# Kernel optimization log

Measured on AMD Instinct MI355X. Metric: run time of the kernel, lower is better.

## Reference

```python
import jax, jax.numpy as jnp
import numpy as np

NUM_VOXELS = 1_000_000
N_POINTS = 1_500_000
TOTAL_PROP_PTS = 1_000_000
NUM_PROPOSALS = 2048
IN_CH = 134  # 3 + 3 + 128
M = 16       # backbone output width
BATCH = 8


def setup_inputs() -> dict:
    key = jax.random.key(0)
    k1, k2, k3, k4, k5, k6 = jax.random.split(key, 6)
    voxel_feats = jax.random.normal(k1, (NUM_VOXELS, IN_CH), dtype=jnp.float32)
    W = jax.random.normal(k2, (IN_CH, M), dtype=jnp.float32) * 0.05
    p2v_map = jax.random.randint(k3, (N_POINTS,), 0, NUM_VOXELS, dtype=jnp.int64)
    # column 0: proposal id (unused), column 1: point index into pt_feats
    col1 = jax.random.randint(k4, (TOTAL_PROP_PTS,), 0, N_POINTS, dtype=jnp.int64)
    gt_proposals_idx = jnp.stack([jnp.zeros_like(col1), col1], axis=1)
    interior = jnp.sort(jax.random.randint(k5, (NUM_PROPOSALS - 1,), 0, TOTAL_PROP_PTS, dtype=jnp.int64))
    gt_proposals_offset = jnp.concatenate([
        jnp.zeros((1,), jnp.int64), interior,
        jnp.full((1,), TOTAL_PROP_PTS, jnp.int64)])
    # column 0 is the batch (scene) id
    locs_scaled = jax.random.randint(k6, (N_POINTS, 4), 0, BATCH, dtype=jnp.int32)
    return {
        'voxel_feats': voxel_feats,
        'W': W,
        'p2v_map': p2v_map,
        'gt_proposals_idx': gt_proposals_idx,
        'gt_proposals_offset': gt_proposals_offset,
        'locs_scaled': locs_scaled,
    }


def reference(voxel_feats, W, p2v_map, gt_proposals_idx, gt_proposals_offset, locs_scaled):
    # Stand-in for the Minkowski sparse backbone: pointwise projection + ReLU, 134 -> 16.
    feats = jax.nn.relu(voxel_feats @ W)                 # (V, 16)
    pt_feats = feats[p2v_map]                            # (N, 16) voxel->point gather

    P = gt_proposals_offset.shape[0] - 1
    point_idx = gt_proposals_idx[:, 1]                   # (T,)
    T = point_idx.shape[0]

    # CSR offsets -> segment ids (replaces the Python loop over proposals)
    seg_ids = jnp.searchsorted(gt_proposals_offset, jnp.arange(T), side='right') - 1

    gathered = pt_feats[point_idx]                       # (T, 16) ragged gather
    sums = jax.ops.segment_sum(gathered, seg_ids, num_segments=P)
    counts = jax.ops.segment_sum(jnp.ones((T,), feats.dtype), seg_ids, num_segments=P)
    proposal_feats = sums / jnp.maximum(counts, 1.0)[:, None]   # (P, 16) segment mean

    batch_idxs = locs_scaled[:, 0]                       # (N,) scene ids
    proposals_batchId = batch_idxs[point_idx][gt_proposals_offset[:-1]]  # (P,)
    proposal_objectness_scores = jnp.ones((P,), dtype=bool)
    return proposal_feats, proposals_batchId, proposal_objectness_scores
```

## Files before the change

### kernel.cpp

```cpp
#include <hip/hip_runtime.h>

#define NUM_VOXELS     1000000
#define N_POINTS       1500000
#define TOTAL_PROP_PTS 1000000
#define NUM_PROPOSALS  2048
#define IN_CH          134
#define M_OUT          16

typedef unsigned int  uint;
typedef unsigned short ushort;

__device__ __forceinline__ ushort f2bf(float f) {
    uint u = __float_as_uint(f);
    uint r = (u + 0x7FFFu + ((u >> 16) & 1u)) >> 16;
    return (ushort)r;
}

__global__ void k_zero_flags(uint* __restrict__ flags4) {
    int i = blockIdx.x * 256 + threadIdx.x;
    if (i < NUM_VOXELS / 4) flags4[i] = 0;
}

__global__ void k_set_flags(const int* __restrict__ prop_idx,
                            const int* __restrict__ p2v,
                            unsigned char* __restrict__ flags) {
    int t = blockIdx.x * 256 + threadIdx.x;
    if (t < TOTAL_PROP_PTS) {
        int p = prop_idx[2 * t + 1];
        flags[p2v[p]] = 1;
    }
}

__global__ __launch_bounds__(256, 2) void k_gemm_relu(
    const float* __restrict__ A, const float* __restrict__ W,
    const unsigned char* __restrict__ flags,
    uint* __restrict__ featsb)
{
    __shared__ float lds[4][64 * 65];
    const int wave = threadIdx.x >> 6;
    const int lane = threadIdx.x & 63;
    const int v0   = blockIdx.x * 256 + wave * 64;
    if (v0 >= NUM_VOXELS) return;

    const int myflag = flags[v0 + lane];

    float* chunk = lds[wave];
    float acc[M_OUT];
#pragma unroll
    for (int c = 0; c < M_OUT; ++c) acc[c] = 0.f;

    for (int kc = 0; kc < IN_CH; kc += 64) {
        const int KC = (IN_CH - kc) >= 64 ? 64 : (IN_CH - kc);
        if (KC == 64) {
            const int half = lane >> 5;
            const int c2   = (lane & 31) * 2;
#pragma unroll 8
            for (int j = 0; j < 32; ++j) {
                const int row = j * 2 + half;
                const int rf  = __shfl(myflag, row, 64);
                if (rf) {
                    const float2 val = *(const float2*)(A + (size_t)(v0 + row) * IN_CH + kc + c2);
                    chunk[row * 65 + c2]     = val.x;
                    chunk[row * 65 + c2 + 1] = val.y;
                }
            }
        } else {
#pragma unroll
            for (int j = 0; j < 6; ++j) {
                const int e   = j * 64 + lane;
                const int row = e / 6;
                const int col = e - row * 6;
                const int rf  = __shfl(myflag, row, 64);
                if (rf) chunk[row * 65 + col] = A[(size_t)(v0 + row) * IN_CH + kc + col];
            }
        }
        const float* wbase = W + kc * M_OUT;
        for (int kk = 0; kk < KC; ++kk) {
            const float a = chunk[lane * 65 + kk];
            const float* wr = wbase + kk * M_OUT;
#pragma unroll
            for (int c = 0; c < M_OUT; ++c) acc[c] = fmaf(a, wr[c], acc[c]);
        }
    }

    if (myflag) {
        uint u[8];
#pragma unroll
        for (int i = 0; i < 8; ++i) {
            const float lo = fmaxf(acc[2 * i],     0.f);
            const float hi = fmaxf(acc[2 * i + 1], 0.f);
            u[i] = (uint)f2bf(lo) | ((uint)f2bf(hi) << 16);
        }
        uint4* orow = (uint4*)(featsb + (size_t)(v0 + lane) * 8);
        orow[0] = make_uint4(u[0], u[1], u[2], u[3]);
        orow[1] = make_uint4(u[4], u[5], u[6], u[7]);
    }
}

__global__ __launch_bounds__(256) void k_propmean(
    const uint*  __restrict__ featsb,
    const int*   __restrict__ p2v,
    const int*   __restrict__ prop_idx,
    const int*   __restrict__ offsets,
    const int*   __restrict__ locs,
    float*       __restrict__ out)
{
    const int s   = blockIdx.x;
    const int tid = threadIdx.x;
    const int t0  = offsets[s];
    const int t1  = offsets[s + 1];

    float acc[M_OUT];
#pragma unroll
    for (int c = 0; c < M_OUT; ++c) acc[c] = 0.f;

    for (int t = t0 + tid; t < t1; t += 256) {
        const int p = prop_idx[2 * t + 1];
        const int v = p2v[p];
        const uint4* fp = (const uint4*)(featsb + (size_t)v * 8);
        const uint4 q0 = fp[0], q1 = fp[1];
        const uint u[8] = {q0.x, q0.y, q0.z, q0.w, q1.x, q1.y, q1.z, q1.w};
#pragma unroll
        for (int i = 0; i < 8; ++i) {
            acc[2 * i]     += __uint_as_float(u[i] << 16);
            acc[2 * i + 1] += __uint_as_float(u[i] & 0xFFFF0000u);
        }
    }

#pragma unroll
    for (int c = 0; c < M_OUT; ++c) {
#pragma unroll
        for (int off = 32; off > 0; off >>= 1)
            acc[c] += __shfl_down(acc[c], off, 64);
    }

    __shared__ float red[4][M_OUT];
    const int lane = tid & 63, wv = tid >> 6;
    if (lane == 0) {
#pragma unroll
        for (int c = 0; c < M_OUT; ++c) red[wv][c] = acc[c];
    }
    __syncthreads();

    if (tid < M_OUT) {
        const float sum = red[0][tid] + red[1][tid] + red[2][tid] + red[3][tid];
        const float cnt = (float)(t1 - t0);
        out[s * M_OUT + tid] = sum / fmaxf(cnt, 1.f);
    }
    if (tid == 0) {
        const int p = prop_idx[2 * t0 + 1];
        out[NUM_PROPOSALS * M_OUT + s]                 = (float)locs[4 * p];
        out[NUM_PROPOSALS * M_OUT + NUM_PROPOSALS + s] = 1.0f;
    }
}

extern "C" void kernel_launch(void* const* d_in, const int* in_sizes, int n_in,
                              void* d_out, int out_size, void* d_ws, size_t ws_size,
                              hipStream_t stream)
{
    const float* A    = (const float*)d_in[0];
    const float* W    = (const float*)d_in[1];
    const int*   p2v  = (const int*)  d_in[2];
    const int*   pidx = (const int*)  d_in[3];
    const int*   offs = (const int*)  d_in[4];
    const int*   locs = (const int*)  d_in[5];
    float*       out  = (float*)      d_out;

    uint*          featsb = (uint*)d_ws;
    unsigned char* flags  = (unsigned char*)d_ws + (size_t)NUM_VOXELS * 32;

    k_zero_flags<<<(NUM_VOXELS / 4 + 255) / 256, 256, 0, stream>>>((uint*)flags);
    k_set_flags<<<(TOTAL_PROP_PTS + 255) / 256, 256, 0, stream>>>(pidx, p2v, flags);
    k_gemm_relu<<<(NUM_VOXELS + 255) / 256, 256, 0, stream>>>(A, W, flags, featsb);
    k_propmean<<<NUM_PROPOSALS, 256, 0, stream>>>(featsb, p2v, pidx, offs, locs, out);
}
```

Baseline: 940.1 us.

## Compact flagged voxels and compute GEMM per-thread rows without LDS staging

Result: no change. 931.3 us (-0.9%).

```diff
diff --git a/kernel.cpp b/kernel.cpp
--- a/kernel.cpp
+++ b/kernel.cpp
@@ -7,7 +7,7 @@
 #define IN_CH          134
 #define M_OUT          16
 
-typedef unsigned int  uint;
+typedef unsigned int   uint;
 typedef unsigned short ushort;
 
 __device__ __forceinline__ ushort f2bf(float f) {
@@ -16,9 +16,10 @@
     return (ushort)r;
 }
 
-__global__ void k_zero_flags(uint* __restrict__ flags4) {
+__global__ void k_zero(uint* __restrict__ flags4, int* __restrict__ count) {
     int i = blockIdx.x * 256 + threadIdx.x;
     if (i < NUM_VOXELS / 4) flags4[i] = 0;
+    if (i == 0) *count = 0;
 }
 
 __global__ void k_set_flags(const int* __restrict__ prop_idx,
@@ -31,59 +32,66 @@
     }
 }
 
-__global__ __launch_bounds__(256, 2) void k_gemm_relu(
+__global__ __launch_bounds__(256) void k_compact(
+    const unsigned char* __restrict__ flags,
+    int* __restrict__ ids, int* __restrict__ count)
+{
+    const int i    = blockIdx.x * 256 + threadIdx.x;
+    const int lane = threadIdx.x & 63;
+    const int f    = (i < NUM_VOXELS) ? (int)flags[i] : 0;
+    const unsigned long long m = __ballot(f);
+    const int cnt = __popcll(m);
+    int base = 0;
+    if (lane == 0 && cnt) base = atomicAdd(count, cnt);
+    base = __shfl(base, 0, 64);
+    if (f) {
+        const unsigned long long lt = m & ((1ull << lane) - 1ull);
+        ids[base + __popcll(lt)] = i;
+    }
+}
+
+__global__ __launch_bounds__(256, 4) void k_gemm_relu(
     const float* __restrict__ A, const float* __restrict__ W,
-    const unsigned char* __restrict__ flags,
+    const int* __restrict__ ids, const int* __restrict__ count,
     uint* __restrict__ featsb)
 {
-    __shared__ float lds[4][64 * 65];
-    const int wave = threadIdx.x >> 6;
-    const int lane = threadIdx.x & 63;
-    const int v0   = blockIdx.x * 256 + wave * 64;
-    if (v0 >= NUM_VOXELS) return;
+    const int cnt = *count;
+    const int idx = blockIdx.x * 256 + threadIdx.x;
+    if ((idx & ~63) >= cnt) return;
+    const int  slot = (idx < cnt) ? idx : (cnt - 1);
+    const int  vid  = ids[slot];
+    const float2* __restrict__ row = (const float2*)(A + (size_t)vid * IN_CH);
 
-    const int myflag = flags[v0 + lane];
-
-    float* chunk = lds[wave];
     float acc[M_OUT];
 #pragma unroll
     for (int c = 0; c < M_OUT; ++c) acc[c] = 0.f;
 
-    for (int kc = 0; kc < IN_CH; kc += 64) {
-        const int KC = (IN_CH - kc) >= 64 ? 64 : (IN_CH - kc);
-        if (KC == 64) {
-            const int half = lane >> 5;
-            const int c2   = (lane & 31) * 2;
-#pragma unroll 8
-            for (int j = 0; j < 32; ++j) {
-                const int row = j * 2 + half;
-                const int rf  = __shfl(myflag, row, 64);
-                if (rf) {
-                    const float2 val = *(const float2*)(A + (size_t)(v0 + row) * IN_CH + kc + c2);
-                    chunk[row * 65 + c2]     = val.x;
-                    chunk[row * 65 + c2 + 1] = val.y;
-                }
-            }
-        } else {
+    for (int ch = 0; ch < 8; ++ch) {
+        float2 b[8];
 #pragma unroll
-            for (int j = 0; j < 6; ++j) {
-                const int e   = j * 64 + lane;
-                const int row = e / 6;
-                const int col = e - row * 6;
-                const int rf  = __shfl(myflag, row, 64);
-                if (rf) chunk[row * 65 + col] = A[(size_t)(v0 + row) * IN_CH + kc + col];
+        for (int j = 0; j < 8; ++j) b[j] = row[ch * 8 + j];
+        const float* __restrict__ wb = W + ch * 16 * M_OUT;
+#pragma unroll
+        for (int j = 0; j < 8; ++j) {
+#pragma unroll
+            for (int c = 0; c < M_OUT; ++c) {
+                acc[c] = fmaf(b[j].x, wb[(2 * j)     * M_OUT + c], acc[c]);
+                acc[c] = fmaf(b[j].y, wb[(2 * j + 1) * M_OUT + c], acc[c]);
             }
         }
-        const float* wbase = W + kc * M_OUT;
-        for (int kk = 0; kk < KC; ++kk) {
-            const float a = chunk[lane * 65 + kk];
-            const float* wr = wbase + kk * M_OUT;
+    }
+    {
+        float2 t0 = row[64], t1 = row[65], t2 = row[66];
+        const float a[6] = {t0.x, t0.y, t1.x, t1.y, t2.x, t2.y};
+        const float* __restrict__ wb = W + 128 * M_OUT;
 #pragma unroll
-            for (int c = 0; c < M_OUT; ++c) acc[c] = fmaf(a, wr[c], acc[c]);
-        }
+        for (int k = 0; k < 6; ++k)
+#pragma unroll
+            for (int c = 0; c < M_OUT; ++c)
+                acc[c] = fmaf(a[k], wb[k * M_OUT + c], acc[c]);
     }
 
-    if (myflag) {
+    if (idx < cnt) {
         uint u[8];
 #pragma unroll
         for (int i = 0; i < 8; ++i) {
@@ -91,7 +99,7 @@
             const float hi = fmaxf(acc[2 * i + 1], 0.f);
             u[i] = (uint)f2bf(lo) | ((uint)f2bf(hi) << 16);
         }
-        uint4* orow = (uint4*)(featsb + (size_t)(v0 + lane) * 8);
+        uint4* orow = (uint4*)(featsb + (size_t)vid * 8);
         orow[0] = make_uint4(u[0], u[1], u[2], u[3]);
         orow[1] = make_uint4(u[4], u[5], u[6], u[7]);
     }
@@ -166,11 +174,15 @@
     const int*   locs = (const int*)  d_in[5];
     float*       out  = (float*)      d_out;
 
-    uint*          featsb = (uint*)d_ws;
-    unsigned char* flags  = (unsigned char*)d_ws + (size_t)NUM_VOXELS * 32;
+    char* ws = (char*)d_ws;
+    uint*          featsb = (uint*)ws;
+    unsigned char* flags  = (unsigned char*)(ws + (size_t)32 * 1024 * 1024);
+    int*           count  = (int*)(ws + (size_t)33 * 1024 * 1024);
+    int*           ids    = (int*)(ws + (size_t)33 * 1024 * 1024 + 1024);
 
-    k_zero_flags<<<(NUM_VOXELS / 4 + 255) / 256, 256, 0, stream>>>((uint*)flags);
+    k_zero     <<<(NUM_VOXELS / 4 + 255) / 256, 256, 0, stream>>>((uint*)flags, count);
     k_set_flags<<<(TOTAL_PROP_PTS + 255) / 256, 256, 0, stream>>>(pidx, p2v, flags);
-    k_gemm_relu<<<(NUM_VOXELS + 255) / 256, 256, 0, stream>>>(A, W, flags, featsb);
-    k_propmean<<<NUM_PROPOSALS, 256, 0, stream>>>(featsb, p2v, pidx, offs, locs, out);
+    k_compact  <<<(NUM_VOXELS + 255) / 256, 256, 0, stream>>>(flags, ids, count);
+    k_gemm_relu<<<(NUM_VOXELS + 255) / 256, 256, 0, stream>>>(A, W, ids, count, featsb);
+    k_propmean <<<NUM_PROPOSALS, 256, 0, stream>>>(featsb, p2v, pidx, offs, locs, out);
 }
```
